# Kernel tuning notes

Hardware: AMD Instinct MI355X
Metric: run time of the kernel (lower is better)

The kernel has to match this reference:

```python
import jax, jax.numpy as jnp
import numpy as np

DIM = 512
HID = DIM // 4        # cross-attention inner dim
MLP_HID = int(DIM * 2.0)
EPS = 1e-5


def _xavier(key, shape):
    fan_in, fan_out = shape[0], shape[1]
    limit = float(np.sqrt(6.0 / (fan_in + fan_out)))
    return jax.random.uniform(key, shape, jnp.float32, -limit, limit)


def setup_inputs() -> dict:
    key = jax.random.key(0)
    ks = jax.random.split(key, 12)
    n, v = 8, 2048
    x = jax.random.normal(ks[0], (n, v, DIM), jnp.float32)
    y = jax.random.normal(ks[1], (n, v, DIM), jnp.float32)
    Wq = _xavier(ks[2], (DIM, HID))
    Wk = _xavier(ks[3], (DIM, HID))
    Wv = _xavier(ks[4], (DIM, DIM))
    gamma = jnp.ones((DIM,), jnp.float32)
    beta = jnp.zeros((DIM,), jnp.float32)
    # nn.Linear default init: U(-1/sqrt(fan_in), 1/sqrt(fan_in))
    b1lim = 1.0 / np.sqrt(DIM)
    W1 = jax.random.uniform(ks[5], (DIM, MLP_HID), jnp.float32, -b1lim, b1lim)
    b1 = jax.random.uniform(ks[6], (MLP_HID,), jnp.float32, -b1lim, b1lim)
    b2lim = 1.0 / np.sqrt(MLP_HID)
    W2 = jax.random.uniform(ks[7], (MLP_HID, DIM), jnp.float32, -b2lim, b2lim)
    b2 = jax.random.uniform(ks[8], (DIM,), jnp.float32, -b2lim, b2lim)
    return {"x": x, "y": y, "Wq": Wq, "Wk": Wk, "Wv": Wv,
            "gamma": gamma, "beta": beta, "W1": W1, "b1": b1, "W2": W2, "b2": b2}


def _layernorm(x, gamma, beta):
    mu = jnp.mean(x, axis=-1, keepdims=True)
    var = jnp.var(x, axis=-1, keepdims=True)
    return (x - mu) * jax.lax.rsqrt(var + EPS) * gamma + beta


def reference(x, y, Wq, Wk, Wv, gamma, beta, W1, b1, W2, b2):
    scale = HID ** (-0.5)
    q = jnp.einsum('nvc,co->nvo', x, Wq)          # [n, q, HID]
    k = jnp.einsum('nvc,co->nvo', y, Wk)          # [n, k, HID]
    v = jnp.einsum('nvc,co->nvo', y, Wv)          # [n, k, DIM]
    attn = jax.nn.softmax(jnp.einsum('nqc,nkc->nqk', q, k) * scale, axis=-1)
    x = x + jnp.einsum('nqk,nkc->nqc', attn, v)   # residual + attention
    h = _layernorm(x, gamma, beta)
    h = jax.nn.gelu(h @ W1 + b1, approximate=False) @ W2 + b2
    return x + h
```

## Files before the change

### kernel.cpp

```cpp
#include <hip/hip_runtime.h>
#include <cstddef>
#include <cstdint>

typedef __attribute__((ext_vector_type(8))) short short8;
typedef __attribute__((ext_vector_type(4))) short s16x4;
typedef __attribute__((ext_vector_type(4))) float f32x4;
typedef __attribute__((ext_vector_type(16))) float f32x16;

#define GLOAD_LDS16(gp, lp) __builtin_amdgcn_global_load_lds( \
    (const __attribute__((address_space(1))) void*)(gp),      \
    (__attribute__((address_space(3))) void*)(lp), 16, 0, 0)

__device__ __forceinline__ short f2bf(float f) {
    union { float f; unsigned u; } v; v.f = f;
    unsigned r = v.u + 0x7fffu + ((v.u >> 16) & 1u);
    return (short)(r >> 16);
}

__device__ __forceinline__ void transpose_tile_f32(
    const float* __restrict__ in, short* __restrict__ out,
    int R, int C, int ty, int tx)
{
    __shared__ short tile[64][68];
    int r0 = ty * 64, c0 = tx * 64;
    int t = threadIdx.x, tr = t >> 6, tc = t & 63;
#pragma unroll
    for (int i = 0; i < 16; ++i) {
        int r = i * 4 + tr;
        tile[r][tc] = f2bf(in[(size_t)(r0 + r) * C + (c0 + tc)]);
    }
    __syncthreads();
#pragma unroll
    for (int i = 0; i < 16; ++i) {
        int r = i * 4 + tr;
        out[(size_t)(c0 + r) * R + (r0 + tc)] = tile[tc][r];
    }
}

__global__ __launch_bounds__(256) void prep_kernel(
    const float* __restrict__ x, const float* __restrict__ y,
    const float* __restrict__ Wq, const float* __restrict__ Wk,
    const float* __restrict__ Wv, const float* __restrict__ W1,
    const float* __restrict__ W2,
    short* xb, short* yb,
    short* WqT, short* WkT, short* WvT, short* W1T, short* W2T)
{
    int bid = blockIdx.x, t = threadIdx.x;
    if (bid < 8192) {
        size_t e = ((size_t)bid << 11) + (size_t)t * 8;
        const float* src; short* dst; size_t o2;
        if (e < 8388608) { src = x; dst = xb; o2 = e; }
        else             { src = y; dst = yb; o2 = e - 8388608; }
        f32x4 a = *(const f32x4*)(src + o2);
        f32x4 b = *(const f32x4*)(src + o2 + 4);
        short8 v;
        v[0] = f2bf(a[0]); v[1] = f2bf(a[1]); v[2] = f2bf(a[2]); v[3] = f2bf(a[3]);
        v[4] = f2bf(b[0]); v[5] = f2bf(b[1]); v[6] = f2bf(b[2]); v[7] = f2bf(b[3]);
        *(short8*)(dst + o2) = v;
        return;
    }
    int b2 = bid - 8192;
    const float* in; short* out; int R, C;
    if (b2 < 16)       { in = Wq; out = WqT; R = 512;  C = 128; }
    else if (b2 < 32)  { in = Wk; out = WkT; R = 512;  C = 128;  b2 -= 16; }
    else if (b2 < 96)  { in = Wv; out = WvT; R = 512;  C = 512;  b2 -= 32; }
    else if (b2 < 224) { in = W1; out = W1T; R = 512;  C = 1024; b2 -= 96; }
    else               { in = W2; out = W2T; R = 1024; C = 512;  b2 -= 224; }
    int nx = C >> 6;
    transpose_tile_f32(in, out, R, C, b2 / nx, b2 % nx);
}

__global__ __launch_bounds__(256, 2) void proj_gemm(
    const short* __restrict__ xb, const short* __restrict__ yb,
    const short* __restrict__ WqT, const short* __restrict__ WkT,
    const short* __restrict__ WvT,
    short* __restrict__ qbf, short* __restrict__ kbff, short* __restrict__ vbf)
{
    __shared__ short As[128][64];
    __shared__ short Bs[128][64];
    int bid = blockIdx.x;
    const short* A; const short* BT; short* outp; int n0, N, mode, mb;
    if (bid < 128)      { A = xb; BT = WqT; outp = qbf;  n0 = 0; N = 128; mode = 0; mb = bid; }
    else if (bid < 256) { A = yb; BT = WkT; outp = kbff; n0 = 0; N = 128; mode = 0; mb = bid - 128; }
    else { int v2 = bid - 256; A = yb; BT = WvT; outp = vbf; n0 = (v2 & 3) << 7; N = 512; mode = 1; mb = v2 >> 2; }
    const int m0 = mb << 7;
    const int K = 512;
    const int t = threadIdx.x, l = t & 63, w = t >> 6;
    const int wm = w >> 1, wn = w & 1;
    const int lo = l & 15, hi = l >> 4;

    f32x4 acc[4][4] = {};
    const int srow = l >> 3;
    const int scg  = (l & 7) ^ (srow & 7);

    for (int kt = 0; kt < K; kt += 64) {
#pragma unroll
        for (int i = 0; i < 4; ++i) {
            int seg = w * 4 + i;
            int row = seg * 8 + srow;
            GLOAD_LDS16(A + (size_t)(m0 + row) * K + kt + scg * 8, &As[seg * 8][0]);
        }
#pragma unroll
        for (int i = 0; i < 4; ++i) {
            int seg = w * 4 + i;
            int row = seg * 8 + srow;
            GLOAD_LDS16(BT + (size_t)(n0 + row) * K + kt + scg * 8, &Bs[seg * 8][0]);
        }
        __syncthreads();
#pragma unroll
        for (int kk = 0; kk < 2; ++kk) {
            short8 af[4], bfv[4];
            const int rc = ((kk * 4 + hi) ^ (lo & 7)) * 8;
#pragma unroll
            for (int mi = 0; mi < 4; ++mi)
                af[mi] = *(const short8*)&As[wm * 64 + mi * 16 + lo][rc];
#pragma unroll
            for (int ni = 0; ni < 4; ++ni)
                bfv[ni] = *(const short8*)&Bs[wn * 64 + ni * 16 + lo][rc];
            __builtin_amdgcn_s_setprio(1);
#pragma unroll
            for (int mi = 0; mi < 4; ++mi)
#pragma unroll
                for (int ni = 0; ni < 4; ++ni)
                    acc[mi][ni] = __builtin_amdgcn_mfma_f32_16x16x32_bf16(
                        af[mi], bfv[ni], acc[mi][ni], 0, 0, 0);
            __builtin_amdgcn_s_setprio(0);
        }
        __syncthreads();
    }

    if (mode == 0) {
#pragma unroll
        for (int mi = 0; mi < 4; ++mi) {
#pragma unroll
            for (int ni = 0; ni < 4; ++ni) {
                int rowb = m0 + wm * 64 + mi * 16 + hi * 4;
                int col  = n0 + wn * 64 + ni * 16 + lo;
                size_t base = ((size_t)(rowb >> 5) * (N >> 4) + (col >> 4)) * 512
                            + ((col & 15) >> 3) * 256 + (rowb & 31) * 8 + (col & 7);
#pragma unroll
                for (int r = 0; r < 4; ++r)
                    outp[base + r * 8] = f2bf(acc[mi][ni][r]);
            }
        }
    } else {
#pragma unroll
        for (int mi = 0; mi < 4; ++mi) {
#pragma unroll
            for (int ni = 0; ni < 4; ++ni) {
                int rowb = m0 + wm * 64 + mi * 16 + hi * 4;
                int col  = n0 + wn * 64 + ni * 16 + lo;
                size_t base = ((size_t)(rowb >> 4) * (N >> 5) + (col >> 5)) * 512
                            + ((rowb & 15) >> 3) * 256 + (col & 31) * 8 + (rowb & 7);
                s16x4 pk;
#pragma unroll
                for (int r = 0; r < 4; ++r) pk[r] = f2bf(acc[mi][ni][r]);
                *(s16x4*)(outp + base) = pk;
            }
        }
    }
}

template<int EPI>
__global__ __launch_bounds__(256, 2) void gemm_kernel(
    const short* __restrict__ A, const short* __restrict__ BT, void* outv,
    const float* __restrict__ bias, const float* __restrict__ resid,
    int N, int K)
{
    __shared__ short As[128][64];
    __shared__ short Bs[128][64];
    int bid = blockIdx.x;
    const int cpx = gridDim.x >> 3;
    bid = (bid & 7) * cpx + (bid >> 3);
    const int nb = N >> 7;
    const int m0 = (bid / nb) << 7;
    const int n0 = (bid % nb) << 7;
    const int t = threadIdx.x, l = t & 63, w = t >> 6;
    const int wm = w >> 1, wn = w & 1;
    const int lo = l & 15, hi = l >> 4;

    f32x4 acc[4][4] = {};
    const int srow = l >> 3;
    const int scg  = (l & 7) ^ (srow & 7);

    for (int kt = 0; kt < K; kt += 64) {
#pragma unroll
        for (int i = 0; i < 4; ++i) {
            int seg = w * 4 + i;
            int row = seg * 8 + srow;
            GLOAD_LDS16(A + (size_t)(m0 + row) * K + kt + scg * 8, &As[seg * 8][0]);
        }
#pragma unroll
        for (int i = 0; i < 4; ++i) {
            int seg = w * 4 + i;
            int row = seg * 8 + srow;
            GLOAD_LDS16(BT + (size_t)(n0 + row) * K + kt + scg * 8, &Bs[seg * 8][0]);
        }
        __syncthreads();
#pragma unroll
        for (int kk = 0; kk < 2; ++kk) {
            short8 af[4], bfv[4];
            const int rc = ((kk * 4 + hi) ^ (lo & 7)) * 8;
#pragma unroll
            for (int mi = 0; mi < 4; ++mi)
                af[mi] = *(const short8*)&As[wm * 64 + mi * 16 + lo][rc];
#pragma unroll
            for (int ni = 0; ni < 4; ++ni)
                bfv[ni] = *(const short8*)&Bs[wn * 64 + ni * 16 + lo][rc];
            __builtin_amdgcn_s_setprio(1);
#pragma unroll
            for (int mi = 0; mi < 4; ++mi)
#pragma unroll
                for (int ni = 0; ni < 4; ++ni)
                    acc[mi][ni] = __builtin_amdgcn_mfma_f32_16x16x32_bf16(
                        af[mi], bfv[ni], acc[mi][ni], 0, 0, 0);
            __builtin_amdgcn_s_setprio(0);
        }
        __syncthreads();
    }

#pragma unroll
    for (int mi = 0; mi < 4; ++mi) {
#pragma unroll
        for (int ni = 0; ni < 4; ++ni) {
#pragma unroll
            for (int r = 0; r < 4; ++r) {
                int row = m0 + wm * 64 + mi * 16 + hi * 4 + r;
                int col = n0 + wn * 64 + ni * 16 + lo;
                size_t idx = (size_t)row * N + col;
                float v = acc[mi][ni][r];
                if (EPI == 2) {
                    v += bias[col];
                    v = 0.5f * v * (1.0f + erff(v * 0.70710678118654752f));
                    ((short*)outv)[idx] = f2bf(v);
                } else {
                    v += bias[col] + resid[idx];
                    ((float*)outv)[idx] = v;
                }
            }
        }
    }
}

__global__ __launch_bounds__(512, 2) void flash_kernel(
    const float* __restrict__ x,
    const short* __restrict__ qbf,
    const short* __restrict__ kbff,
    const short* __restrict__ vbf,
    float* __restrict__ xres,
    const float* __restrict__ gamma,
    const float* __restrict__ beta,
    short* __restrict__ hb)
{
    __shared__ short Ps[2][2][8][512];
    __shared__ float mpart[2][8][32];
    __shared__ float lpart[8][32];
    __shared__ float rsum[8][64];
    __shared__ float rsq[8][64];
    __shared__ float murs[2][64];

    const int bid = blockIdx.x;
    const int n = bid & 7;
    const int qtile = bid >> 3;
    const int q0 = qtile << 6;
    const int t = threadIdx.x, l = t & 63, w = t >> 6;
    const int qh = w >> 2, kq = w & 3;
    const int lo5 = l & 31, hi2 = l >> 5;
    const float C1 = 0.08838834764831845f * 1.4426950408889634f;
    const float THR = 90.509668f;

    short8 qf[8];
    {
        const short* qp = qbf + (((size_t)(n * 64 + qtile * 2 + qh) * 8) << 9) + l * 8;
#pragma unroll
        for (int s = 0; s < 8; ++s) qf[s] = *(const short8*)(qp + (s << 9));
    }

    f32x16 o00 = {}, o01 = {}, o10 = {}, o11 = {};
    float m0 = -1e30f, m1 = -1e30f, lp = 0.f;
    float ac0 = 0.f, ac1 = 0.f;

    const short* kb0 = kbff + (((size_t)(n * 64) * 8) << 9);
    const short* vb0 = vbf + ((((size_t)(n * 128)) * 16 + w * 2) << 9);

    {
        const short* kp = kb0 + (((size_t)kq * 8) << 9) + l * 8;
        short8 kf[8];
#pragma unroll
        for (int s = 0; s < 8; ++s) kf[s] = *(const short8*)(kp + (s << 9));
        f32x16 sa = {};
        __builtin_amdgcn_s_setprio(1);
#pragma unroll
        for (int s = 0; s < 8; ++s)
            sa = __builtin_amdgcn_mfma_f32_32x32x16_bf16(kf[s], qf[s], sa, 0, 0, 0);
        __builtin_amdgcn_s_setprio(0);
        float lmax = sa[0];
#pragma unroll
        for (int r = 1; r < 16; ++r) lmax = fmaxf(lmax, sa[r]);
        lmax = fmaxf(lmax, __shfl_xor(lmax, 32));
        if (l < 32) mpart[0][w][l] = lmax;
        __syncthreads();
        m0 = fmaxf(fmaxf(mpart[0][0][lo5], mpart[0][1][lo5]),
                   fmaxf(mpart[0][2][lo5], mpart[0][3][lo5]));
        m1 = fmaxf(fmaxf(mpart[0][4][lo5], mpart[0][5][lo5]),
                   fmaxf(mpart[0][6][lo5], mpart[0][7][lo5]));
        const float mC1 = (qh ? m1 : m0) * C1;
        float lsum = 0.f;
#pragma unroll
        for (int r = 0; r < 16; ++r) {
            float p = exp2f(fmaf(sa[r], C1, -mC1));
            sa[r] = p; lsum += p;
        }
        lp = lsum;
        int wq[8], sx[8];
#pragma unroll
        for (int q2 = 0; q2 < 8; ++q2) {
            int a;
            asm("v_cvt_pk_bf16_f32 %0, %1, %2"
                : "=v"(a) : "v"(sa[2 * q2]), "v"(sa[2 * q2 + 1]));
            wq[q2] = a;
        }
#pragma unroll
        for (int q2 = 0; q2 < 8; ++q2) sx[q2] = __shfl_xor(wq[q2], 32);
        union { int i[4]; short8 v; } u0, u1;
        u0.i[0] = hi2 ? sx[2] : wq[0];
        u0.i[1] = hi2 ? sx[3] : wq[1];
        u0.i[2] = hi2 ? wq[2] : sx[0];
        u0.i[3] = hi2 ? wq[3] : sx[1];
        u1.i[0] = hi2 ? sx[6] : wq[4];
        u1.i[1] = hi2 ? sx[7] : wq[5];
        u1.i[2] = hi2 ? wq[6] : sx[4];
        u1.i[3] = hi2 ? wq[7] : sx[5];
        *(short8*)&Ps[0][qh][kq * 2][l * 8]     = u0.v;
        *(short8*)&Ps[0][qh][kq * 2 + 1][l * 8] = u1.v;
    }

    for (int kt2 = 0; kt2 < 16; ++kt2) {
        const bool hn = kt2 < 15;
        const short* vp = vb0 + (((size_t)(kt2 * 128)) << 9) + l * 8;

        short8 vfa[8];
#pragma unroll
        for (int p = 0; p < 8; ++p)
            vfa[p] = *(const short8*)(vp + (((size_t)((p >> 1) * 16 + (p & 1))) << 9));

        f32x16 sa;
        float an0 = 1.f, an1 = 1.f;
        if (hn) {
            const short* kp = kb0 + (((size_t)((kt2 + 1) * 4 + kq) * 8) << 9) + l * 8;
            short8 kf[8];
#pragma unroll
            for (int s = 0; s < 8; ++s) kf[s] = *(const short8*)(kp + (s << 9));
            f32x16 z = {};
            sa = z;
            __builtin_amdgcn_s_setprio(1);
#pragma unroll
            for (int s = 0; s < 8; ++s)
                sa = __builtin_amdgcn_mfma_f32_32x32x16_bf16(kf[s], qf[s], sa, 0, 0, 0);
            __builtin_amdgcn_s_setprio(0);
            float lmax = sa[0];
#pragma unroll
            for (int r = 1; r < 16; ++r) lmax = fmaxf(lmax, sa[r]);
            lmax = fmaxf(lmax, __shfl_xor(lmax, 32));
            if (l < 32) mpart[(kt2 + 1) & 1][w][l] = lmax;
        }
        __syncthreads();

        short8 vfb[8];
#pragma unroll
        for (int p = 0; p < 8; ++p)
            vfb[p] = *(const short8*)(vp + (((size_t)((4 + (p >> 1)) * 16 + (p & 1))) << 9));

        if (hn) {
            const int mb = (kt2 + 1) & 1;
            float nm0 = fmaxf(fmaxf(mpart[mb][0][lo5], mpart[mb][1][lo5]),
                              fmaxf(mpart[mb][2][lo5], mpart[mb][3][lo5]));
            float nm1 = fmaxf(fmaxf(mpart[mb][4][lo5], mpart[mb][5][lo5]),
                              fmaxf(mpart[mb][6][lo5], mpart[mb][7][lo5]));
            float t0 = (nm0 > m0 + THR) ? nm0 : m0;
            float t1 = (nm1 > m1 + THR) ? nm1 : m1;
            an0 = exp2f((m0 - t0) * C1);
            an1 = exp2f((m1 - t1) * C1);
            m0 = t0; m1 = t1;
            const float mC1 = (qh ? m1 : m0) * C1;
            float lsum = 0.f;
#pragma unroll
            for (int r = 0; r < 16; ++r) {
                float p = exp2f(fmaf(sa[r], C1, -mC1));
                sa[r] = p; lsum += p;
            }
            lp = lp * (qh ? an1 : an0) + lsum;
        }

        if (!(__all(ac0 == 1.f) & __all(ac1 == 1.f))) {
#pragma unroll
            for (int r = 0; r < 16; ++r) {
                int qr = (r & 3) + 8 * (r >> 2) + 4 * hi2;
                float ar0 = __shfl(ac0, qr);
                float ar1 = __shfl(ac1, qr);
                o00[r] *= ar0; o01[r] *= ar0;
                o10[r] *= ar1; o11[r] *= ar1;
            }
        }

        const int pb = kt2 & 1;
        __builtin_amdgcn_s_setprio(1);
#pragma unroll
        for (int ks = 0; ks < 4; ++ks) {
            short8 p0 = *(const short8*)&Ps[pb][0][ks][l * 8];
            short8 p1 = *(const short8*)&Ps[pb][1][ks][l * 8];
            o00 = __builtin_amdgcn_mfma_f32_32x32x16_bf16(p0, vfa[ks * 2 + 0], o00, 0, 0, 0);
            o01 = __builtin_amdgcn_mfma_f32_32x32x16_bf16(p0, vfa[ks * 2 + 1], o01, 0, 0, 0);
            o10 = __builtin_amdgcn_mfma_f32_32x32x16_bf16(p1, vfa[ks * 2 + 0], o10, 0, 0, 0);
            o11 = __builtin_amdgcn_mfma_f32_32x32x16_bf16(p1, vfa[ks * 2 + 1], o11, 0, 0, 0);
        }
#pragma unroll
        for (int ks = 4; ks < 8; ++ks) {
            short8 p0 = *(const short8*)&Ps[pb][0][ks][l * 8];
            short8 p1 = *(const short8*)&Ps[pb][1][ks][l * 8];
            o00 = __builtin_amdgcn_mfma_f32_32x32x16_bf16(p0, vfb[(ks - 4) * 2 + 0], o00, 0, 0, 0);
            o01 = __builtin_amdgcn_mfma_f32_32x32x16_bf16(p0, vfb[(ks - 4) * 2 + 1], o01, 0, 0, 0);
            o10 = __builtin_amdgcn_mfma_f32_32x32x16_bf16(p1, vfb[(ks - 4) * 2 + 0], o10, 0, 0, 0);
            o11 = __builtin_amdgcn_mfma_f32_32x32x16_bf16(p1, vfb[(ks - 4) * 2 + 1], o11, 0, 0, 0);
        }
        __builtin_amdgcn_s_setprio(0);

        if (hn) {
            int wq[8], sx[8];
#pragma unroll
            for (int q2 = 0; q2 < 8; ++q2) {
                int a;
                asm("v_cvt_pk_bf16_f32 %0, %1, %2"
                    : "=v"(a) : "v"(sa[2 * q2]), "v"(sa[2 * q2 + 1]));
                wq[q2] = a;
            }
#pragma unroll
            for (int q2 = 0; q2 < 8; ++q2) sx[q2] = __shfl_xor(wq[q2], 32);
            union { int i[4]; short8 v; } u0, u1;
            u0.i[0] = hi2 ? sx[2] : wq[0];
            u0.i[1] = hi2 ? sx[3] : wq[1];
            u0.i[2] = hi2 ? wq[2] : sx[0];
            u0.i[3] = hi2 ? wq[3] : sx[1];
            u1.i[0] = hi2 ? sx[6] : wq[4];
            u1.i[1] = hi2 ? sx[7] : wq[5];
            u1.i[2] = hi2 ? wq[6] : sx[4];
            u1.i[3] = hi2 ? wq[7] : sx[5];
            const int nb2 = (kt2 + 1) & 1;
            *(short8*)&Ps[nb2][qh][kq * 2][l * 8]     = u0.v;
            *(short8*)&Ps[nb2][qh][kq * 2 + 1][l * 8] = u1.v;
            ac0 = an0; ac1 = an1;
        }
    }

    float l2 = lp + __shfl_xor(lp, 32);
    if (l < 32) lpart[w][l] = l2;
    __syncthreads();
    float li0 = 1.f / (lpart[0][lo5] + lpart[1][lo5] + lpart[2][lo5] + lpart[3][lo5]);
    float li1 = 1.f / (lpart[4][lo5] + lpart[5][lo5] + lpart[6][lo5] + lpart[7][lo5]);
    const int c0 = w * 64 + lo5;
#pragma unroll
    for (int r = 0; r < 16; ++r) {
        int qr = (r & 3) + 8 * (r >> 2) + 4 * hi2;
        float ir0 = __shfl(li0, qr);
        float ir1 = __shfl(li1, qr);
        size_t b0 = ((size_t)(n * 2048 + q0 + qr) << 9) + c0;
        size_t b1 = ((size_t)(n * 2048 + q0 + 32 + qr) << 9) + c0;
        float v00 = x[b0]      + o00[r] * ir0;
        float v01 = x[b0 + 32] + o01[r] * ir0;
        float v10 = x[b1]      + o10[r] * ir1;
        float v11 = x[b1 + 32] + o11[r] * ir1;
        xres[b0] = v00; xres[b0 + 32] = v01;
        xres[b1] = v10; xres[b1 + 32] = v11;
        o00[r] = v00; o01[r] = v01; o10[r] = v10; o11[r] = v11;
        float s0 = v00 + v01, sq0 = v00 * v00 + v01 * v01;
        float s1 = v10 + v11, sq1 = v10 * v10 + v11 * v11;
#pragma unroll
        for (int mm = 1; mm < 32; mm <<= 1) {
            s0 += __shfl_xor(s0, mm); sq0 += __shfl_xor(sq0, mm);
            s1 += __shfl_xor(s1, mm); sq1 += __shfl_xor(sq1, mm);
        }
        if (lo5 == 0) {
            rsum[w][qr] = s0;      rsq[w][qr] = sq0;
            rsum[w][32 + qr] = s1; rsq[w][32 + qr] = sq1;
        }
    }
    __syncthreads();
    if (t < 64) {
        float s = 0.f, qq = 0.f;
#pragma unroll
        for (int ww = 0; ww < 8; ++ww) { s += rsum[ww][t]; qq += rsq[ww][t]; }
        float mu = s * (1.0f / 512.0f);
        float var = qq * (1.0f / 512.0f) - mu * mu;
        murs[0][t] = mu;
        murs[1][t] = rsqrtf(var + 1e-5f);
    }
    __syncthreads();
    const float g0 = gamma[c0], g1 = gamma[c0 + 32];
    const float e0 = beta[c0],  e1 = beta[c0 + 32];
#pragma unroll
    for (int r = 0; r < 16; ++r) {
        int qr = (r & 3) + 8 * (r >> 2) + 4 * hi2;
        float mu0 = murs[0][qr],      rs0 = murs[1][qr];
        float mu1 = murs[0][32 + qr], rs1 = murs[1][32 + qr];
        size_t h0 = ((size_t)(n * 2048 + q0 + qr) << 9) + c0;
        size_t h1 = ((size_t)(n * 2048 + q0 + 32 + qr) << 9) + c0;
        hb[h0]      = f2bf((o00[r] - mu0) * rs0 * g0 + e0);
        hb[h0 + 32] = f2bf((o01[r] - mu0) * rs0 * g1 + e1);
        hb[h1]      = f2bf((o10[r] - mu1) * rs1 * g0 + e0);
        hb[h1 + 32] = f2bf((o11[r] - mu1) * rs1 * g1 + e1);
    }
}

extern "C" void kernel_launch(void* const* d_in, const int* in_sizes, int n_in,
                              void* d_out, int out_size, void* d_ws, size_t ws_size,
                              hipStream_t stream)
{
    const float* x     = (const float*)d_in[0];
    const float* y     = (const float*)d_in[1];
    const float* Wq    = (const float*)d_in[2];
    const float* Wk    = (const float*)d_in[3];
    const float* Wv    = (const float*)d_in[4];
    const float* gamma = (const float*)d_in[5];
    const float* beta  = (const float*)d_in[6];
    const float* W1    = (const float*)d_in[7];
    const float* b1    = (const float*)d_in[8];
    const float* W2    = (const float*)d_in[9];
    const float* b2    = (const float*)d_in[10];
    float* out = (float*)d_out;

    char* ws = (char*)d_ws;
    size_t off = 0;
    auto alloc = [&](size_t bytes) -> void* {
        void* p = ws + off;
        off += (bytes + 255) & ~(size_t)255;
        return p;
    };
    short* WqT  = (short*)alloc((size_t)128 * 512 * 2);
    short* WkT  = (short*)alloc((size_t)128 * 512 * 2);
    short* WvT  = (short*)alloc((size_t)512 * 512 * 2);
    short* W1T  = (short*)alloc((size_t)1024 * 512 * 2);
    short* W2T  = (short*)alloc((size_t)512 * 1024 * 2);
    short* qbf  = (short*)alloc((size_t)16384 * 128 * 2);
    short* kbff = (short*)alloc((size_t)16384 * 128 * 2);
    short* vbf  = (short*)alloc((size_t)16384 * 512 * 2);
    short* xb   = (short*)alloc((size_t)16384 * 512 * 2);
    short* hb   = xb;
    short* yb   = (short*)alloc((size_t)16384 * 512 * 2);
    short* gb   = (short*)alloc((size_t)16384 * 1024 * 2);

    prep_kernel<<<8544, 256, 0, stream>>>(x, y, Wq, Wk, Wv, W1, W2,
                                          xb, yb, WqT, WkT, WvT, W1T, W2T);
    proj_gemm<<<768, 256, 0, stream>>>(xb, yb, WqT, WkT, WvT, qbf, kbff, vbf);
    flash_kernel<<<256, 512, 0, stream>>>(x, qbf, kbff, vbf, out, gamma, beta, hb);
    gemm_kernel<2><<<1024, 256, 0, stream>>>(hb, W1T, gb, b1, nullptr, 1024, 512);
    gemm_kernel<3><<<512,  256, 0, stream>>>(gb, W2T, out, b2, out, 512, 1024);

    (void)in_sizes; (void)n_in; (void)out_size; (void)ws_size;
}
```

Before: 172.1 us.

## Fuse fp32-to-bf16 input conversion into projection GEMM and prefetch K in flash loop

```diff
diff --git a/kernel.cpp b/kernel.cpp
--- a/kernel.cpp
+++ b/kernel.cpp
@@ -17,49 +17,14 @@
     return (short)(r >> 16);
 }
 
-__device__ __forceinline__ void transpose_tile_f32(
-    const float* __restrict__ in, short* __restrict__ out,
-    int R, int C, int ty, int tx)
-{
-    __shared__ short tile[64][68];
-    int r0 = ty * 64, c0 = tx * 64;
-    int t = threadIdx.x, tr = t >> 6, tc = t & 63;
-#pragma unroll
-    for (int i = 0; i < 16; ++i) {
-        int r = i * 4 + tr;
-        tile[r][tc] = f2bf(in[(size_t)(r0 + r) * C + (c0 + tc)]);
-    }
-    __syncthreads();
-#pragma unroll
-    for (int i = 0; i < 16; ++i) {
-        int r = i * 4 + tr;
-        out[(size_t)(c0 + r) * R + (r0 + tc)] = tile[tc][r];
-    }
-}
-
 __global__ __launch_bounds__(256) void prep_kernel(
-    const float* __restrict__ x, const float* __restrict__ y,
     const float* __restrict__ Wq, const float* __restrict__ Wk,
     const float* __restrict__ Wv, const float* __restrict__ W1,
     const float* __restrict__ W2,
-    short* xb, short* yb,
     short* WqT, short* WkT, short* WvT, short* W1T, short* W2T)
 {
-    int bid = blockIdx.x, t = threadIdx.x;
-    if (bid < 8192) {
-        size_t e = ((size_t)bid << 11) + (size_t)t * 8;
-        const float* src; short* dst; size_t o2;
-        if (e < 8388608) { src = x; dst = xb; o2 = e; }
-        else             { src = y; dst = yb; o2 = e - 8388608; }
-        f32x4 a = *(const f32x4*)(src + o2);
-        f32x4 b = *(const f32x4*)(src + o2 + 4);
-        short8 v;
-        v[0] = f2bf(a[0]); v[1] = f2bf(a[1]); v[2] = f2bf(a[2]); v[3] = f2bf(a[3]);
-        v[4] = f2bf(b[0]); v[5] = f2bf(b[1]); v[6] = f2bf(b[2]); v[7] = f2bf(b[3]);
-        *(short8*)(dst + o2) = v;
-        return;
-    }
-    int b2 = bid - 8192;
+    __shared__ short tile[64][68];
+    int b2 = blockIdx.x;
     const float* in; short* out; int R, C;
     if (b2 < 16)       { in = Wq; out = WqT; R = 512;  C = 128; }
     else if (b2 < 32)  { in = Wk; out = WkT; R = 512;  C = 128;  b2 -= 16; }
@@ -67,11 +32,23 @@
     else if (b2 < 224) { in = W1; out = W1T; R = 512;  C = 1024; b2 -= 96; }
     else               { in = W2; out = W2T; R = 1024; C = 512;  b2 -= 224; }
     int nx = C >> 6;
-    transpose_tile_f32(in, out, R, C, b2 / nx, b2 % nx);
+    int r0 = (b2 / nx) * 64, c0 = (b2 % nx) * 64;
+    int t = threadIdx.x, tr = t >> 6, tc = t & 63;
+#pragma unroll
+    for (int i = 0; i < 16; ++i) {
+        int r = i * 4 + tr;
+        tile[r][tc] = f2bf(in[(size_t)(r0 + r) * C + (c0 + tc)]);
+    }
+    __syncthreads();
+#pragma unroll
+    for (int i = 0; i < 16; ++i) {
+        int r = i * 4 + tr;
+        out[(size_t)(c0 + r) * R + (r0 + tc)] = tile[tc][r];
+    }
 }
 
 __global__ __launch_bounds__(256, 2) void proj_gemm(
-    const short* __restrict__ xb, const short* __restrict__ yb,
+    const float* __restrict__ x, const float* __restrict__ y,
     const short* __restrict__ WqT, const short* __restrict__ WkT,
     const short* __restrict__ WvT,
     short* __restrict__ qbf, short* __restrict__ kbff, short* __restrict__ vbf)
@@ -79,10 +56,10 @@
     __shared__ short As[128][64];
     __shared__ short Bs[128][64];
     int bid = blockIdx.x;
-    const short* A; const short* BT; short* outp; int n0, N, mode, mb;
-    if (bid < 128)      { A = xb; BT = WqT; outp = qbf;  n0 = 0; N = 128; mode = 0; mb = bid; }
-    else if (bid < 256) { A = yb; BT = WkT; outp = kbff; n0 = 0; N = 128; mode = 0; mb = bid - 128; }
-    else { int v2 = bid - 256; A = yb; BT = WvT; outp = vbf; n0 = (v2 & 3) << 7; N = 512; mode = 1; mb = v2 >> 2; }
+    const float* A; const short* BT; short* outp; int n0, N, mode, mb;
+    if (bid < 128)      { A = x; BT = WqT; outp = qbf;  n0 = 0; N = 128; mode = 0; mb = bid; }
+    else if (bid < 256) { A = y; BT = WkT; outp = kbff; n0 = 0; N = 128; mode = 0; mb = bid - 128; }
+    else { int v2 = bid - 256; A = y; BT = WvT; outp = vbf; n0 = (v2 & 3) << 7; N = 512; mode = 1; mb = v2 >> 2; }
     const int m0 = mb << 7;
     const int K = 512;
     const int t = threadIdx.x, l = t & 63, w = t >> 6;
@@ -98,13 +75,23 @@
         for (int i = 0; i < 4; ++i) {
             int seg = w * 4 + i;
             int row = seg * 8 + srow;
-            GLOAD_LDS16(A + (size_t)(m0 + row) * K + kt + scg * 8, &As[seg * 8][0]);
+            GLOAD_LDS16(BT + (size_t)(n0 + row) * K + kt + scg * 8, &Bs[seg * 8][0]);
         }
 #pragma unroll
         for (int i = 0; i < 4; ++i) {
-            int seg = w * 4 + i;
-            int row = seg * 8 + srow;
-            GLOAD_LDS16(BT + (size_t)(n0 + row) * K + kt + scg * 8, &Bs[seg * 8][0]);
+            int c = i * 256 + t;
+            int row = c >> 3, ch = c & 7;
+            const float* src = A + (size_t)(m0 + row) * K + kt + ch * 8;
+            f32x4 u0 = *(const f32x4*)src;
+            f32x4 u1 = *(const f32x4*)(src + 4);
+            int d0, d1, d2, d3;
+            asm("v_cvt_pk_bf16_f32 %0, %1, %2" : "=v"(d0) : "v"(u0[0]), "v"(u0[1]));
+            asm("v_cvt_pk_bf16_f32 %0, %1, %2" : "=v"(d1) : "v"(u0[2]), "v"(u0[3]));
+            asm("v_cvt_pk_bf16_f32 %0, %1, %2" : "=v"(d2) : "v"(u1[0]), "v"(u1[1]));
+            asm("v_cvt_pk_bf16_f32 %0, %1, %2" : "=v"(d3) : "v"(u1[2]), "v"(u1[3]));
+            union { int i[4]; short8 v; } uu;
+            uu.i[0] = d0; uu.i[1] = d1; uu.i[2] = d2; uu.i[3] = d3;
+            *(short8*)&As[row][((ch ^ (row & 7)) * 8)] = uu.v;
         }
         __syncthreads();
 #pragma unroll
@@ -278,14 +265,15 @@
 
     f32x16 o00 = {}, o01 = {}, o10 = {}, o11 = {};
     float m0 = -1e30f, m1 = -1e30f, lp = 0.f;
-    float ac0 = 0.f, ac1 = 0.f;
+    float ac0 = 1.f, ac1 = 1.f;
 
     const short* kb0 = kbff + (((size_t)(n * 64) * 8) << 9);
     const short* vb0 = vbf + ((((size_t)(n * 128)) * 16 + w * 2) << 9);
 
+    short8 kf[8];
+
     {
         const short* kp = kb0 + (((size_t)kq * 8) << 9) + l * 8;
-        short8 kf[8];
 #pragma unroll
         for (int s = 0; s < 8; ++s) kf[s] = *(const short8*)(kp + (s << 9));
         f32x16 sa = {};
@@ -294,6 +282,11 @@
         for (int s = 0; s < 8; ++s)
             sa = __builtin_amdgcn_mfma_f32_32x32x16_bf16(kf[s], qf[s], sa, 0, 0, 0);
         __builtin_amdgcn_s_setprio(0);
+        {
+            const short* kp1 = kb0 + (((size_t)(4 + kq) * 8) << 9) + l * 8;
+#pragma unroll
+            for (int s = 0; s < 8; ++s) kf[s] = *(const short8*)(kp1 + (s << 9));
+        }
         float lmax = sa[0];
 #pragma unroll
         for (int r = 1; r < 16; ++r) lmax = fmaxf(lmax, sa[r]);
@@ -347,10 +340,6 @@
         f32x16 sa;
         float an0 = 1.f, an1 = 1.f;
         if (hn) {
-            const short* kp = kb0 + (((size_t)((kt2 + 1) * 4 + kq) * 8) << 9) + l * 8;
-            short8 kf[8];
-#pragma unroll
-            for (int s = 0; s < 8; ++s) kf[s] = *(const short8*)(kp + (s << 9));
             f32x16 z = {};
             sa = z;
             __builtin_amdgcn_s_setprio(1);
@@ -358,6 +347,13 @@
             for (int s = 0; s < 8; ++s)
                 sa = __builtin_amdgcn_mfma_f32_32x32x16_bf16(kf[s], qf[s], sa, 0, 0, 0);
             __builtin_amdgcn_s_setprio(0);
+        }
+        if (kt2 + 2 < 16) {
+            const short* kp = kb0 + (((size_t)((kt2 + 2) * 4 + kq) * 8) << 9) + l * 8;
+#pragma unroll
+            for (int s = 0; s < 8; ++s) kf[s] = *(const short8*)(kp + (s << 9));
+        }
+        if (hn) {
             float lmax = sa[0];
 #pragma unroll
             for (int r = 1; r < 16; ++r) lmax = fmaxf(lmax, sa[r]);
@@ -365,7 +361,6 @@
             if (l < 32) mpart[(kt2 + 1) & 1][w][l] = lmax;
         }
         __syncthreads();
-
         short8 vfb[8];
 #pragma unroll
         for (int p = 0; p < 8; ++p)
@@ -390,42 +385,7 @@
                 sa[r] = p; lsum += p;
             }
             lp = lp * (qh ? an1 : an0) + lsum;
-        }
-
-        if (!(__all(ac0 == 1.f) & __all(ac1 == 1.f))) {
-#pragma unroll
-            for (int r = 0; r < 16; ++r) {
-                int qr = (r & 3) + 8 * (r >> 2) + 4 * hi2;
-                float ar0 = __shfl(ac0, qr);
-                float ar1 = __shfl(ac1, qr);
-                o00[r] *= ar0; o01[r] *= ar0;
-                o10[r] *= ar1; o11[r] *= ar1;
-            }
-        }
-
-        const int pb = kt2 & 1;
-        __builtin_amdgcn_s_setprio(1);
-#pragma unroll
-        for (int ks = 0; ks < 4; ++ks) {
-            short8 p0 = *(const short8*)&Ps[pb][0][ks][l * 8];
-            short8 p1 = *(const short8*)&Ps[pb][1][ks][l * 8];
-            o00 = __builtin_amdgcn_mfma_f32_32x32x16_bf16(p0, vfa[ks * 2 + 0], o00, 0, 0, 0);
-            o01 = __builtin_amdgcn_mfma_f32_32x32x16_bf16(p0, vfa[ks * 2 + 1], o01, 0, 0, 0);
-            o10 = __builtin_amdgcn_mfma_f32_32x32x16_bf16(p1, vfa[ks * 2 + 0], o10, 0, 0, 0);
-            o11 = __builtin_amdgcn_mfma_f32_32x32x16_bf16(p1, vfa[ks * 2 + 1], o11, 0, 0, 0);
-        }
-#pragma unroll
-        for (int ks = 4; ks < 8; ++ks) {
-            short8 p0 = *(const short8*)&Ps[pb][0][ks][l * 8];
-            short8 p1 = *(const short8*)&Ps[pb][1][ks][l * 8];
-            o00 = __builtin_amdgcn_mfma_f32_32x32x16_bf16(p0, vfb[(ks - 4) * 2 + 0], o00, 0, 0, 0);
-            o01 = __builtin_amdgcn_mfma_f32_32x32x16_bf16(p0, vfb[(ks - 4) * 2 + 1], o01, 0, 0, 0);
-            o10 = __builtin_amdgcn_mfma_f32_32x32x16_bf16(p1, vfb[(ks - 4) * 2 + 0], o10, 0, 0, 0);
-            o11 = __builtin_amdgcn_mfma_f32_32x32x16_bf16(p1, vfb[(ks - 4) * 2 + 1], o11, 0, 0, 0);
-        }
-        __builtin_amdgcn_s_setprio(0);
-
-        if (hn) {
+
             int wq[8], sx[8];
 #pragma unroll
             for (int q2 = 0; q2 < 8; ++q2) {
@@ -448,8 +408,39 @@
             const int nb2 = (kt2 + 1) & 1;
             *(short8*)&Ps[nb2][qh][kq * 2][l * 8]     = u0.v;
             *(short8*)&Ps[nb2][qh][kq * 2 + 1][l * 8] = u1.v;
-            ac0 = an0; ac1 = an1;
-        }
+        }
+        if (!(__all(ac0 == 1.f) & __all(ac1 == 1.f))) {
+#pragma unroll
+            for (int r = 0; r < 16; ++r) {
+                int qr = (r & 3) + 8 * (r >> 2) + 4 * hi2;
+                float ar0 = __shfl(ac0, qr);
+                float ar1 = __shfl(ac1, qr);
+                o00[r] *= ar0; o01[r] *= ar0;
+                o10[r] *= ar1; o11[r] *= ar1;
+            }
+        }
+        const int pb = kt2 & 1;
+        __builtin_amdgcn_s_setprio(1);
+#pragma unroll
+        for (int ks = 0; ks < 4; ++ks) {
+            short8 p0 = *(const short8*)&Ps[pb][0][ks][l * 8];
+            short8 p1 = *(const short8*)&Ps[pb][1][ks][l * 8];
+            o00 = __builtin_amdgcn_mfma_f32_32x32x16_bf16(p0, vfa[ks * 2 + 0], o00, 0, 0, 0);
+            o01 = __builtin_amdgcn_mfma_f32_32x32x16_bf16(p0, vfa[ks * 2 + 1], o01, 0, 0, 0);
+            o10 = __builtin_amdgcn_mfma_f32_32x32x16_bf16(p1, vfa[ks * 2 + 0], o10, 0, 0, 0);
+            o11 = __builtin_amdgcn_mfma_f32_32x32x16_bf16(p1, vfa[ks * 2 + 1], o11, 0, 0, 0);
+        }
+#pragma unroll
+        for (int ks = 4; ks < 8; ++ks) {
+            short8 p0 = *(const short8*)&Ps[pb][0][ks][l * 8];
+            short8 p1 = *(const short8*)&Ps[pb][1][ks][l * 8];
+            o00 = __builtin_amdgcn_mfma_f32_32x32x16_bf16(p0, vfb[(ks - 4) * 2 + 0], o00, 0, 0, 0);
+            o01 = __builtin_amdgcn_mfma_f32_32x32x16_bf16(p0, vfb[(ks - 4) * 2 + 1], o01, 0, 0, 0);
+            o10 = __builtin_amdgcn_mfma_f32_32x32x16_bf16(p1, vfb[(ks - 4) * 2 + 0], o10, 0, 0, 0);
+            o11 = __builtin_amdgcn_mfma_f32_32x32x16_bf16(p1, vfb[(ks - 4) * 2 + 1], o11, 0, 0, 0);
+        }
+        __builtin_amdgcn_s_setprio(0);
+        ac0 = an0; ac1 = an1;
     }
 
     float l2 = lp + __shfl_xor(lp, 32);
@@ -543,14 +534,12 @@
     short* qbf  = (short*)alloc((size_t)16384 * 128 * 2);
     short* kbff = (short*)alloc((size_t)16384 * 128 * 2);
     short* vbf  = (short*)alloc((size_t)16384 * 512 * 2);
-    short* xb   = (short*)alloc((size_t)16384 * 512 * 2);
-    short* hb   = xb;
-    short* yb   = (short*)alloc((size_t)16384 * 512 * 2);
+    short* hb   = (short*)alloc((size_t)16384 * 512 * 2);
     short* gb   = (short*)alloc((size_t)16384 * 1024 * 2);
 
-    prep_kernel<<<8544, 256, 0, stream>>>(x, y, Wq, Wk, Wv, W1, W2,
-                                          xb, yb, WqT, WkT, WvT, W1T, W2T);
-    proj_gemm<<<768, 256, 0, stream>>>(xb, yb, WqT, WkT, WvT, qbf, kbff, vbf);
+    prep_kernel<<<352, 256, 0, stream>>>(Wq, Wk, Wv, W1, W2,
+                                         WqT, WkT, WvT, W1T, W2T);
+    proj_gemm<<<768, 256, 0, stream>>>(x, y, WqT, WkT, WvT, qbf, kbff, vbf);
     flash_kernel<<<256, 512, 0, stream>>>(x, qbf, kbff, vbf, out, gamma, beta, hb);
     gemm_kernel<2><<<1024, 256, 0, stream>>>(hb, W1T, gb, b1, nullptr, 1024, 512);
     gemm_kernel<3><<<512,  256, 0, stream>>>(gb, W2T, out, b2, out, 512, 1024);
```

After: 174.5 us. No clear change (+1.4%).
